# Kernel tuning notes

Measured on AMD Instinct MI355X. Metric: run time of the kernel, lower is better.

Reference implementation:

```python
import jax, jax.numpy as jnp
import numpy as np

NPOINT = 1024
RADII = (0.1, 0.2)
NSAMPLES = (32, 64)
BN_EPS = 1e-5


def _fps(xyz, npoint):
    # furthest point sampling; xyz (B,N,3) -> idx (B,npoint) int32
    B, N, _ = xyz.shape
    def step(carry, _):
        dist, last = carry
        last_pt = jnp.take_along_axis(xyz, last[:, None, None], axis=1)  # (B,1,3)
        d = jnp.sum((xyz - last_pt) ** 2, axis=-1)                       # (B,N)
        dist = jnp.minimum(dist, d)
        nxt = jnp.argmax(dist, axis=1).astype(jnp.int32)
        return (dist, nxt), nxt
    init = (jnp.full((B, N), 1e10, xyz.dtype), jnp.zeros((B,), jnp.int32))
    _, idxs = jax.lax.scan(step, init, None, length=npoint - 1)
    return jnp.concatenate([jnp.zeros((B, 1), jnp.int32), idxs.T], axis=1)


def _ball_query(radius, nsample, xyz, new_xyz):
    # dense ball query: first `nsample` in-radius point indices, pad with first hit
    N = xyz.shape[1]
    d2 = jnp.sum((new_xyz[:, :, None, :] - xyz[:, None, :, :]) ** 2, -1)  # (B,S,N)
    ar = jnp.arange(N, dtype=jnp.int32)
    order = jnp.where(d2 < radius * radius, ar[None, None, :], N)
    idx = -jax.lax.top_k(-order, nsample)[0]          # ascending smallest indices
    first = idx[..., :1]                              # centroid always within radius
    return jnp.where(idx == N, first, idx)


def _group(points, idx):
    # points (B,N,D), idx (B,S,K) -> (B,S,K,D)
    B, S, K = idx.shape
    flat = idx.reshape(B, S * K)
    return jnp.take_along_axis(points, flat[..., None], axis=1).reshape(B, S, K, points.shape[-1])


def _bn(x, g, b, axes):
    # training-mode batch norm over `axes`, channel-last affine
    m = jnp.mean(x, axes, keepdims=True)
    v = jnp.var(x, axes, keepdims=True)
    return g * (x - m) * jax.lax.rsqrt(v + BN_EPS) + b


def setup_inputs() -> dict:
    key = jax.random.key(0)
    ks = jax.random.split(key, 16)
    B, N, C = 8, 4096, 128
    C_in, C_out, mid = 131, 256, 64   # C_in = C + 3 (use_xyz), mid = C_out // 4
    return {
        "xyz": jax.random.uniform(ks[0], (B, N, 3), jnp.float32),
        "features": jax.random.normal(ks[1], (B, C, N), jnp.float32),
        "W1": jax.random.normal(ks[2], (mid, 10), jnp.float32) * 0.3,
        "b1": jnp.zeros((mid,), jnp.float32),
        "W2": jax.random.normal(ks[3], (C_in, mid), jnp.float32) * 0.1,
        "b2": jnp.zeros((C_in,), jnp.float32),
        "Wcr": jax.random.normal(ks[4], (C_out, C_in), jnp.float32) * 0.1,
        "bcr": jnp.zeros((C_out,), jnp.float32),
        "g_map": jax.random.uniform(ks[5], (2, mid), jnp.float32, 0.5, 1.5),
        "b_map": jax.random.normal(ks[6], (2, mid), jnp.float32) * 0.1,
        "g_rs": jax.random.uniform(ks[7], (2, C_in), jnp.float32, 0.5, 1.5),
        "b_rs": jax.random.normal(ks[8], (2, C_in), jnp.float32) * 0.1,
        "g_cr": jax.random.uniform(ks[9], (2, C_out), jnp.float32, 0.5, 1.5),
        "b_cr": jax.random.normal(ks[10], (2, C_out), jnp.float32) * 0.1,
    }


def reference(xyz, features, W1, b1, W2, b2, Wcr, bcr,
              g_map, b_map, g_rs, b_rs, g_cr, b_cr):
    xyz_sg = jax.lax.stop_gradient(xyz)
    fps_idx = _fps(xyz_sg, NPOINT)                                  # (B,S)
    new_xyz = jnp.take_along_axis(xyz, fps_idx[..., None], axis=1)  # (B,S,3)
    pts_feat = jnp.transpose(features, (0, 2, 1))                   # (B,N,C)
    feats_list = []
    for i, (r, k) in enumerate(zip(RADII, NSAMPLES)):
        idx = _ball_query(r, k, xyz_sg, jax.lax.stop_gradient(new_xyz))
        gx = _group(xyz, idx)                      # (B,S,K,3) abs coords
        rel = gx - new_xyz[:, :, None, :]          # (B,S,K,3) relative coords
        gf = _group(pts_feat, idx)                 # (B,S,K,C)
        dist = jnp.sqrt(jnp.sum(rel * rel, -1, keepdims=True) + 1e-12)
        coord_xi = jnp.broadcast_to(gx[:, :, 0:1, :], gx.shape)
        h = jnp.concatenate([dist, coord_xi, gx, rel], axis=-1)     # (B,S,K,10)
        h = jax.nn.relu(_bn(jnp.einsum('bskc,oc->bsko', h, W1) + b1,
                            g_map[i], b_map[i], (0, 1, 2)))
        h = jnp.einsum('bskc,oc->bsko', h, W2) + b2                 # (B,S,K,C_in)
        x = jnp.concatenate([rel, gf], axis=-1)                     # (B,S,K,C_in)
        x = jax.nn.relu(_bn(h * x, g_rs[i], b_rs[i], (0, 1, 2)))
        x = jnp.max(x, axis=2)                                      # pool over nsample
        x = jax.nn.relu(_bn(jnp.einsum('bsc,oc->bso', x, Wcr) + bcr,
                            g_cr[i], b_cr[i], (0, 1)))              # (B,S,C_out)
        feats_list.append(x)
    feats = jnp.transpose(jnp.concatenate(feats_list, -1), (0, 2, 1))  # (B, 2*C_out, S)
    return new_xyz, feats
```

## Files before the change

kernel.cpp:

```cpp
#include <hip/hip_runtime.h>
#include <math.h>

#define NB 8
#define NN 4096
#define NS 1024
#define NC 128
#define MID 64
#define CIN 131
#define COUT 256
#define PSTRIDE (2048 * 262)
#define SSTRIDE (256 * 512)

template <int N>
__device__ __forceinline__ float dpp_ror(float x) {
  return __int_as_float(
      __builtin_amdgcn_update_dpp(0, __float_as_int(x), 0x120 + N, 0xF, 0xF, false));
}
__device__ __forceinline__ float wave_sum(float v) {
  v += dpp_ror<1>(v); v += dpp_ror<2>(v); v += dpp_ror<4>(v); v += dpp_ror<8>(v);
  v += __shfl_xor(v, 16); v += __shfl_xor(v, 32);
  return v;
}
__device__ __forceinline__ float wave_max64(float v) {
  v = fmaxf(v, dpp_ror<1>(v)); v = fmaxf(v, dpp_ror<2>(v));
  v = fmaxf(v, dpp_ror<4>(v)); v = fmaxf(v, dpp_ror<8>(v));
  v = fmaxf(v, __shfl_xor(v, 16)); v = fmaxf(v, __shfl_xor(v, 32));
  return v;
}
__device__ __forceinline__ void wave_sum4(float& a, float& b, float& c, float& d) {
  a += dpp_ror<1>(a); b += dpp_ror<1>(b); c += dpp_ror<1>(c); d += dpp_ror<1>(d);
  a += dpp_ror<2>(a); b += dpp_ror<2>(b); c += dpp_ror<2>(c); d += dpp_ror<2>(d);
  a += dpp_ror<4>(a); b += dpp_ror<4>(b); c += dpp_ror<4>(c); d += dpp_ror<4>(d);
  a += dpp_ror<8>(a); b += dpp_ror<8>(b); c += dpp_ror<8>(c); d += dpp_ror<8>(d);
  a += __shfl_xor(a, 16); b += __shfl_xor(b, 16); c += __shfl_xor(c, 16); d += __shfl_xor(d, 16);
  a += __shfl_xor(a, 32); b += __shfl_xor(b, 32); c += __shfl_xor(c, 32); d += __shfl_xor(d, 32);
}
__device__ __forceinline__ void wave_max4_32(float& a, float& b, float& c, float& d) {
  a = fmaxf(a, dpp_ror<1>(a)); b = fmaxf(b, dpp_ror<1>(b)); c = fmaxf(c, dpp_ror<1>(c)); d = fmaxf(d, dpp_ror<1>(d));
  a = fmaxf(a, dpp_ror<2>(a)); b = fmaxf(b, dpp_ror<2>(b)); c = fmaxf(c, dpp_ror<2>(c)); d = fmaxf(d, dpp_ror<2>(d));
  a = fmaxf(a, dpp_ror<4>(a)); b = fmaxf(b, dpp_ror<4>(b)); c = fmaxf(c, dpp_ror<4>(c)); d = fmaxf(d, dpp_ror<4>(d));
  a = fmaxf(a, dpp_ror<8>(a)); b = fmaxf(b, dpp_ror<8>(b)); c = fmaxf(c, dpp_ror<8>(c)); d = fmaxf(d, dpp_ror<8>(d));
  a = fmaxf(a, __shfl_xor(a, 16)); b = fmaxf(b, __shfl_xor(b, 16));
  c = fmaxf(c, __shfl_xor(c, 16)); d = fmaxf(d, __shfl_xor(d, 16));
}
__device__ __forceinline__ void wave_max4_64(float& a, float& b, float& c, float& d) {
  wave_max4_32(a, b, c, d);
  a = fmaxf(a, __shfl_xor(a, 32)); b = fmaxf(b, __shfl_xor(b, 32));
  c = fmaxf(c, __shfl_xor(c, 32)); d = fmaxf(d, __shfl_xor(d, 32));
}

__global__ __launch_bounds__(256) void fps_kernel(const float* __restrict__ xyz,
                                                  float* __restrict__ out) {
#pragma clang fp contract(off)
  const int b = blockIdx.x;
  const int tid = threadIdx.x;
  const int lane = tid & 63, w = tid >> 6;
  __shared__ float4 pts[NN];
  __shared__ int sel[NS];
  __shared__ unsigned long long wkey[2][4];
  const float* base = xyz + (size_t)b * NN * 3;
  for (int t = tid; t < NN; t += 256)
    pts[t] = make_float4(base[3 * t], base[3 * t + 1], base[3 * t + 2], 0.f);
  if (tid == 0) sel[0] = 0;
  __syncthreads();
  float px[16], py[16], pz[16], dd[16];
#pragma unroll
  for (int q = 0; q < 16; q++) {
    float4 P = pts[tid * 16 + q];
    px[q] = P.x; py[q] = P.y; pz[q] = P.z; dd[q] = 1e10f;
  }
  float lx = pts[0].x, ly = pts[0].y, lz = pts[0].z;
  for (int it = 1; it < NS; ++it) {
    float bv = -1.0f; int bq = 0;
#pragma unroll
    for (int q = 0; q < 16; q++) {
      float dx = px[q] - lx, dy = py[q] - ly, dz = pz[q] - lz;
      float d2 = dx * dx + dy * dy + dz * dz;
      float dn = fminf(dd[q], d2);
      dd[q] = dn;
      if (dn > bv) { bv = dn; bq = q; }
    }
    const int bi = tid * 16 + bq;
    float wm = wave_max64(bv);
    unsigned long long msk = __ballot(bv == wm);
    int srcl = __ffsll(msk) - 1;
    const int p = it & 1;
    if (lane == srcl)
      wkey[p][w] = ((unsigned long long)__float_as_uint(wm) << 32) | (unsigned)(65535 - bi);
    __syncthreads();
    unsigned long long kk = wkey[p][0];
#pragma unroll
    for (int u = 1; u < 4; u++) {
      unsigned long long o = wkey[p][u];
      if (o > kk) kk = o;
    }
    int li = 65535 - (int)(kk & 0xFFFFu);
    if (tid == 0) sel[it] = li;
    float4 L = pts[li];
    lx = L.x; ly = L.y; lz = L.z;
  }
  __syncthreads();
  for (int s = tid; s < NS; s += 256) {
    float4 P = pts[sel[s]];
    float* o = out + ((size_t)b * NS + s) * 3;
    o[0] = P.x; o[1] = P.y; o[2] = P.z;
  }
}

__global__ void ft_kernel(const float* __restrict__ f, float* __restrict__ ft) {
  __shared__ float tile[32][33];
  int n0 = blockIdx.x * 32, c0 = blockIdx.y * 32, b = blockIdx.z;
  int tx = threadIdx.x, ty = threadIdx.y;
  for (int r = 0; r < 32; r += 8)
    tile[ty + r][tx] = f[((size_t)b * NC + (c0 + ty + r)) * NN + n0 + tx];
  __syncthreads();
  for (int r = 0; r < 32; r += 8)
    ft[((size_t)b * NN + n0 + ty + r) * NC + c0 + tx] = tile[tx][ty + r];
}

__global__ void wcrt_kernel(const float* __restrict__ Wcr, float* __restrict__ wcrT) {
  int t = blockIdx.x * blockDim.x + threadIdx.x;
  if (t >= CIN * COUT) return;
  int c = t % COUT, d = t / COUT;
  wcrT[t] = Wcr[c * CIN + d];
}

__global__ __launch_bounds__(256) void ball_kernel(const float* __restrict__ xyz,
                                                   const float* __restrict__ nxyz,
                                                   int* __restrict__ idx0,
                                                   int* __restrict__ idx1) {
#pragma clang fp contract(off)
  __shared__ float4 pts[NN];
  const int scale = blockIdx.y;
  const int K = scale ? 64 : 32;
  const float r2 = scale ? 0.04f : 0.01f;
  int* __restrict__ idx = scale ? idx1 : idx0;
  const int lane = threadIdx.x & 63, w = threadIdx.x >> 6;
  const int c0 = blockIdx.x * 64;
  const int b = c0 >> 10;
  const float* base = xyz + (size_t)b * NN * 3;
  for (int t = threadIdx.x; t < NN; t += 256)
    pts[t] = make_float4(base[3 * t], base[3 * t + 1], base[3 * t + 2], 0.f);
  __syncthreads();
  const unsigned long long ltmask = (1ull << lane) - 1;
  for (int ci = 0; ci < 16; ci++) {
    const int center = c0 + w * 16 + ci;
    const float cx = nxyz[center * 3], cy = nxyz[center * 3 + 1], cz = nxyz[center * 3 + 2];
    int cnt = 0, first = -1;
    int* o = idx + (size_t)center * K;
    for (int st64 = 0; st64 < 64; st64++) {
      const int j = st64 * 64 + lane;
      float4 P = pts[j];
      float dx = P.x - cx, dy = P.y - cy, dz = P.z - cz;
      float d2 = dx * dx + dy * dy + dz * dz;
      const bool hit = d2 < r2;
      unsigned long long mask = __ballot(hit);
      int pos = cnt + __popcll(mask & ltmask);
      if (hit && pos < K) o[pos] = j;
      if (first < 0 && mask) first = st64 * 64 + __ffsll(mask) - 1;
      cnt += __popcll(mask);
      if (cnt >= K) break;
    }
    if (cnt < K && lane >= cnt && lane < K) o[lane] = first;
  }
}

__global__ __launch_bounds__(256) void p1_kernel(
    const float* __restrict__ xyz, const float* __restrict__ nxyz,
    const int* __restrict__ idx0, const int* __restrict__ idx1,
    const float* __restrict__ W1, const float* __restrict__ b1,
    float* __restrict__ parts) {
  __shared__ float accS[MID], accQ[MID];
  const int scale = blockIdx.y;
  const int nblk = scale ? 2048 : 1024;
  if ((int)blockIdx.x >= nblk) return;
  const int K = scale ? 64 : 32, ksh = scale ? 6 : 5, G = scale ? 1 : 2;
  const int* __restrict__ idx = scale ? idx1 : idx0;
  float* __restrict__ partials = parts + (size_t)scale * PSTRIDE + (size_t)blockIdx.x * (2 * MID);
  const int tid = threadIdx.x, lane = tid & 63, wave = tid >> 6;
  if (tid < MID) { accS[tid] = 0.f; accQ[tid] = 0.f; }
  __syncthreads();
  const int sub = lane >> ksh;
  const int k = lane & (K - 1);
  const int center = blockIdx.x * (4 * G) + wave * G + sub;
  const int b = center >> 10;
  const int* ip = idx + (size_t)center * K;
  const int j = ip[k];
  const int j0 = ip[0];
  const float* xb = xyz + (size_t)b * NN * 3;
  const float gxx = xb[3 * j], gxy = xb[3 * j + 1], gxz = xb[3 * j + 2];
  const float c0x = xb[3 * j0], c0y = xb[3 * j0 + 1], c0z = xb[3 * j0 + 2];
  const float cx = nxyz[center * 3], cy = nxyz[center * 3 + 1], cz = nxyz[center * 3 + 2];
  const float rx = gxx - cx, ry = gxy - cy, rz = gxz - cz;
  const float dst = sqrtf(rx * rx + ry * ry + rz * rz + 1e-12f);
  float h[10] = {dst, c0x, c0y, c0z, gxx, gxy, gxz, rx, ry, rz};
#pragma unroll
  for (int c = 0; c < MID; c += 4) {
    float a0 = b1[c], a1 = b1[c + 1], a2 = b1[c + 2], a3 = b1[c + 3];
    const float* w0 = W1 + c * 10;
    const float* w1 = w0 + 10;
    const float* w2 = w0 + 20;
    const float* w3 = w0 + 30;
#pragma unroll
    for (int d = 0; d < 10; d++) {
      a0 += h[d] * w0[d]; a1 += h[d] * w1[d]; a2 += h[d] * w2[d]; a3 += h[d] * w3[d];
    }
    float v0 = a0, v1 = a1, v2 = a2, v3 = a3;
    wave_sum4(v0, v1, v2, v3);
    float q0 = a0 * a0, q1 = a1 * a1, q2 = a2 * a2, q3 = a3 * a3;
    wave_sum4(q0, q1, q2, q3);
    if (lane == 0) {
      atomicAdd(&accS[c], v0); atomicAdd(&accS[c + 1], v1);
      atomicAdd(&accS[c + 2], v2); atomicAdd(&accS[c + 3], v3);
      atomicAdd(&accQ[c], q0); atomicAdd(&accQ[c + 1], q1);
      atomicAdd(&accQ[c + 2], q2); atomicAdd(&accQ[c + 3], q3);
    }
  }
  __syncthreads();
  for (int t = tid; t < 2 * MID; t += 256)
    partials[t] = (t < MID ? accS[t] : accQ[t - MID]);
}

__global__ __launch_bounds__(256) void red2_kernel(const float* __restrict__ pbase,
                                                   int pstride, int nb0, int nb1,
                                                   double* __restrict__ stats, int obase) {
  __shared__ double red[256];
  const int scale = blockIdx.y;
  const int nblk = scale ? nb1 : nb0;
  const float* part = pbase + (size_t)scale * pstride;
  double* st = stats + scale * 1024;
  const int c = blockIdx.x;
  const int ncol = gridDim.x;
  double a = 0.0;
  for (int r = threadIdx.x; r < nblk; r += 256)
    a += (double)part[(size_t)r * ncol + c];
  red[threadIdx.x] = a;
  __syncthreads();
  for (int s = 128; s > 0; s >>= 1) {
    if (threadIdx.x < s) red[threadIdx.x] += red[threadIdx.x + s];
    __syncthreads();
  }
  if (threadIdx.x == 0) st[obase + c] = red[0];
}

template <bool UFT>
__global__ __launch_bounds__(256) void p2_kernel(
    const float* __restrict__ xyz, const float* __restrict__ nxyz,
    const float* __restrict__ feat, const float* __restrict__ ft,
    const int* __restrict__ idx0, const int* __restrict__ idx1,
    const float* __restrict__ W1, const float* __restrict__ b1,
    const float* __restrict__ W2, const float* __restrict__ b2,
    const float* __restrict__ g_map, const float* __restrict__ b_map,
    const double* __restrict__ stats, float* __restrict__ pm0,
    float* __restrict__ pm1, float* __restrict__ parts) {
  __shared__ float accS[CIN], accQ[CIN];
  __shared__ float sc1[MID], sh1[MID];
  const int scale = blockIdx.y;
  const int nblk = scale ? 2048 : 1024;
  if ((int)blockIdx.x >= nblk) return;
  const int K = scale ? 64 : 32, ksh = scale ? 6 : 5, G = scale ? 1 : 2;
  const int* __restrict__ idx = scale ? idx1 : idx0;
  float* __restrict__ pm = scale ? pm1 : pm0;
  const double* st = stats + scale * 1024;
  const float* g1 = g_map + scale * MID;
  const float* bt1 = b_map + scale * MID;
  float* __restrict__ partials = parts + (size_t)scale * PSTRIDE + (size_t)blockIdx.x * (2 * CIN);
  const int tid = threadIdx.x, lane = tid & 63, wave = tid >> 6;
  for (int t = tid; t < CIN; t += 256) { accS[t] = 0.f; accQ[t] = 0.f; }
  if (tid < MID) {
    const double cnt = (double)NB * NS * K;
    double mean = st[tid] / cnt;
    double var = st[64 + tid] / cnt - mean * mean;
    if (var < 0.0) var = 0.0;
    float is = (float)(1.0 / sqrt(var + 1e-5));
    float sc = g1[tid] * is;
    sc1[tid] = sc;
    sh1[tid] = bt1[tid] - (float)mean * sc;
  }
  __syncthreads();
  const int per = nblk >> 3;
  const int lb = ((int)blockIdx.x & 7) * per + ((int)blockIdx.x >> 3);
  const int sub = lane >> ksh;
  const int k = lane & (K - 1);
  const int center = lb * (4 * G) + wave * G + sub;
  const int b = center >> 10;
  const int* ip = idx + (size_t)center * K;
  const int j = ip[k];
  const int j0 = ip[0];
  const float* xb = xyz + (size_t)b * NN * 3;
  const float gxx = xb[3 * j], gxy = xb[3 * j + 1], gxz = xb[3 * j + 2];
  const float c0x = xb[3 * j0], c0y = xb[3 * j0 + 1], c0z = xb[3 * j0 + 2];
  const float cx = nxyz[center * 3], cy = nxyz[center * 3 + 1], cz = nxyz[center * 3 + 2];
  const float rx = gxx - cx, ry = gxy - cy, rz = gxz - cz;
  const float dst = sqrtf(rx * rx + ry * ry + rz * rz + 1e-12f);
  float h[10] = {dst, c0x, c0y, c0z, gxx, gxy, gxz, rx, ry, rz};
  float t[MID];
#pragma unroll
  for (int c = 0; c < MID; c++) {
    float a = b1[c];
    const float* wp = W1 + c * 10;
#pragma unroll
    for (int d = 0; d < 10; d++) a += h[d] * wp[d];
    t[c] = fmaxf(sc1[c] * a + sh1[c], 0.0f);
  }
  auto chan = [&](int c, float x) {
    float z = b2[c];
    const float4* w4 = reinterpret_cast<const float4*>(W2 + c * MID);
#pragma unroll
    for (int d4 = 0; d4 < MID / 4; d4++) {
      float4 w = w4[d4];
      z += t[4 * d4 + 0] * w.x + t[4 * d4 + 1] * w.y + t[4 * d4 + 2] * w.z + t[4 * d4 + 3] * w.w;
    }
    float p = z * x;
    float v = wave_sum(p);
    float q = wave_sum(p * p);
    if (lane == 0) { atomicAdd(&accS[c], v); atomicAdd(&accQ[c], q); }
    float pmax = p;
    if (K == 64) pmax = wave_max64(pmax);
    else {
      pmax = fmaxf(pmax, dpp_ror<1>(pmax)); pmax = fmaxf(pmax, dpp_ror<2>(pmax));
      pmax = fmaxf(pmax, dpp_ror<4>(pmax)); pmax = fmaxf(pmax, dpp_ror<8>(pmax));
      pmax = fmaxf(pmax, __shfl_xor(pmax, 16));
    }
    if (k == (c & (K - 1))) pm[(size_t)center * CIN + c] = pmax;
  };
  auto chan4 = [&](int c, float x0, float x1, float x2, float x3) {
    const float4* wa = reinterpret_cast<const float4*>(W2 + (size_t)(c + 0) * MID);
    const float4* wb = reinterpret_cast<const float4*>(W2 + (size_t)(c + 1) * MID);
    const float4* wc = reinterpret_cast<const float4*>(W2 + (size_t)(c + 2) * MID);
    const float4* wd = reinterpret_cast<const float4*>(W2 + (size_t)(c + 3) * MID);
    float z0 = b2[c], z1 = b2[c + 1], z2 = b2[c + 2], z3 = b2[c + 3];
#pragma unroll
    for (int d4 = 0; d4 < MID / 4; d4++) {
      float t0 = t[4 * d4 + 0], t1 = t[4 * d4 + 1], t2 = t[4 * d4 + 2], t3 = t[4 * d4 + 3];
      float4 w;
      w = wa[d4]; z0 += t0 * w.x + t1 * w.y + t2 * w.z + t3 * w.w;
      w = wb[d4]; z1 += t0 * w.x + t1 * w.y + t2 * w.z + t3 * w.w;
      w = wc[d4]; z2 += t0 * w.x + t1 * w.y + t2 * w.z + t3 * w.w;
      w = wd[d4]; z3 += t0 * w.x + t1 * w.y + t2 * w.z + t3 * w.w;
    }
    float p0 = z0 * x0, p1 = z1 * x1, p2 = z2 * x2, p3 = z3 * x3;
    float v0 = p0, v1 = p1, v2 = p2, v3 = p3;
    wave_sum4(v0, v1, v2, v3);
    float q0 = p0 * p0, q1 = p1 * p1, q2 = p2 * p2, q3 = p3 * p3;
    wave_sum4(q0, q1, q2, q3);
    if (lane == 0) {
      atomicAdd(&accS[c], v0); atomicAdd(&accS[c + 1], v1);
      atomicAdd(&accS[c + 2], v2); atomicAdd(&accS[c + 3], v3);
      atomicAdd(&accQ[c], q0); atomicAdd(&accQ[c + 1], q1);
      atomicAdd(&accQ[c + 2], q2); atomicAdd(&accQ[c + 3], q3);
    }
    float m0 = p0, m1 = p1, m2 = p2, m3 = p3;
    if (K == 64) wave_max4_64(m0, m1, m2, m3);
    else wave_max4_32(m0, m1, m2, m3);
    if (k == ((c + 0) & (K - 1))) pm[(size_t)center * CIN + c + 0] = m0;
    if (k == ((c + 1) & (K - 1))) pm[(size_t)center * CIN + c + 1] = m1;
    if (k == ((c + 2) & (K - 1))) pm[(size_t)center * CIN + c + 2] = m2;
    if (k == ((c + 3) & (K - 1))) pm[(size_t)center * CIN + c + 3] = m3;
  };
  chan(0, rx); chan(1, ry); chan(2, rz);
  const float4* ftb4 = UFT ? reinterpret_cast<const float4*>(ft + ((size_t)b * NN + j) * NC)
                           : nullptr;
  const float* fb = feat + (size_t)b * NC * NN + j;
  for (int f0 = 0; f0 < NC; f0 += 4) {
    float4 fr;
    if (UFT) {
      fr = ftb4[f0 >> 2];
    } else {
      fr.x = fb[(size_t)f0 * NN]; fr.y = fb[(size_t)(f0 + 1) * NN];
      fr.z = fb[(size_t)(f0 + 2) * NN]; fr.w = fb[(size_t)(f0 + 3) * NN];
    }
    chan4(3 + f0, fr.x, fr.y, fr.z, fr.w);
  }
  __syncthreads();
  for (int t = tid; t < 2 * CIN; t += 256)
    partials[t] = (t < CIN ? accS[t] : accQ[t - CIN]);
}

__global__ __launch_bounds__(256) void s4_kernel(const float* __restrict__ pm0,
                                                 const float* __restrict__ pm1,
                                                 const float* __restrict__ wcrT,
                                                 const float* __restrict__ bcr,
                                                 const float* __restrict__ g_rs,
                                                 const float* __restrict__ b_rs,
                                                 float* __restrict__ feats,
                                                 const double* __restrict__ stats,
                                                 float* __restrict__ spart) {
  __shared__ float xms[16][132];
  __shared__ float sc2[CIN], sh2[CIN];
  const int scale = blockIdx.y;
  const int K = scale ? 64 : 32;
  const float* pm = scale ? pm1 : pm0;
  const double* st = stats + scale * 1024;
  const float* g2 = g_rs + scale * CIN;
  const float* bt2 = b_rs + scale * CIN;
  const int choff = scale << 8;
  float* sp = spart + (size_t)scale * SSTRIDE + (size_t)blockIdx.x * 512;
  const int tid = threadIdx.x;
  if (tid < CIN) {
    const double cnt = (double)NB * NS * K;
    double mean = st[128 + tid] / cnt;
    double var = st[259 + tid] / cnt - mean * mean;
    if (var < 0.0) var = 0.0;
    float is = (float)(1.0 / sqrt(var + 1e-5));
    float sc = g2[tid] * is;
    sc2[tid] = sc;
    sh2[tid] = bt2[tid] - (float)mean * sc;
  }
  float bc = bcr[tid];
  float s1 = 0.f, s2 = 0.f;
  __syncthreads();
  for (int r0 = blockIdx.x * 16; r0 < NB * NS; r0 += gridDim.x * 16) {
    for (int t = tid; t < 16 * CIN; t += 256) {
      int rr = t / CIN, cc = t % CIN;
      xms[rr][cc] = fmaxf(sc2[cc] * pm[(size_t)(r0 + rr) * CIN + cc] + sh2[cc], 0.0f);
    }
    __syncthreads();
    float acc[16];
#pragma unroll
    for (int u = 0; u < 16; u++) acc[u] = bc;
    for (int d4 = 0; d4 < 32; d4++) {
      float w0 = wcrT[(4 * d4 + 0) * COUT + tid];
      float w1 = wcrT[(4 * d4 + 1) * COUT + tid];
      float w2 = wcrT[(4 * d4 + 2) * COUT + tid];
      float w3 = wcrT[(4 * d4 + 3) * COUT + tid];
#pragma unroll
      for (int u = 0; u < 16; u++) {
        float4 xv = *reinterpret_cast<const float4*>(&xms[u][4 * d4]);
        acc[u] += xv.x * w0 + xv.y * w1 + xv.z * w2 + xv.w * w3;
      }
    }
#pragma unroll
    for (int d = 128; d < CIN; d++) {
      float w = wcrT[d * COUT + tid];
#pragma unroll
      for (int u = 0; u < 16; u++) acc[u] += xms[u][d] * w;
    }
#pragma unroll
    for (int u = 0; u < 16; u++) {
      int r = r0 + u;
      int b = r >> 10, s = r & (NS - 1);
      feats[((size_t)b * 512 + choff + tid) * NS + s] = acc[u];
      s1 += acc[u];
      s2 += acc[u] * acc[u];
    }
    __syncthreads();
  }
  sp[tid] = s1;
  sp[256 + tid] = s2;
}

__global__ void s5_kernel(float* __restrict__ feats, const double* __restrict__ stats,
                          const float* __restrict__ g_cr, const float* __restrict__ b_cr) {
  const int scale = blockIdx.y;
  const double* st = stats + scale * 1024;
  int t = blockIdx.x * blockDim.x + threadIdx.x;
  int s = t & (NS - 1);
  int c = (t >> 10) & (COUT - 1);
  int b = t >> 18;
  double mean = st[512 + c] / (double)(NB * NS);
  double var = st[768 + c] / (double)(NB * NS) - mean * mean;
  if (var < 0.0) var = 0.0;
  float is = (float)(1.0 / sqrt(var + 1e-5));
  float sc = g_cr[scale * 256 + c] * is;
  float sh = b_cr[scale * 256 + c] - (float)mean * sc;
  size_t o = ((size_t)b * 512 + scale * 256 + c) * NS + s;
  feats[o] = fmaxf(sc * feats[o] + sh, 0.0f);
}

extern "C" void kernel_launch(void* const* d_in, const int* in_sizes, int n_in,
                              void* d_out, int out_size, void* d_ws, size_t ws_size,
                              hipStream_t stream) {
  const float* xyz  = (const float*)d_in[0];
  const float* feat = (const float*)d_in[1];
  const float* W1   = (const float*)d_in[2];
  const float* b1   = (const float*)d_in[3];
  const float* W2   = (const float*)d_in[4];
  const float* b2   = (const float*)d_in[5];
  const float* Wcr  = (const float*)d_in[6];
  const float* bcr  = (const float*)d_in[7];
  const float* g_map = (const float*)d_in[8];
  const float* b_map = (const float*)d_in[9];
  const float* g_rs  = (const float*)d_in[10];
  const float* b_rs  = (const float*)d_in[11];
  const float* g_cr  = (const float*)d_in[12];
  const float* b_cr  = (const float*)d_in[13];

  char* wsb = (char*)d_ws;
  size_t off = 0;
  auto take = [&](size_t bytes) -> void* {
    void* p = wsb + off;
    off = (off + bytes + 255) & ~(size_t)255;
    return p;
  };
  int*    idxb0 = (int*)take((size_t)NB * NS * 32 * sizeof(int));
  int*    idxb1 = (int*)take((size_t)NB * NS * 64 * sizeof(int));
  float*  pm0   = (float*)take((size_t)NB * NS * CIN * sizeof(float));
  float*  pm1   = (float*)take((size_t)NB * NS * CIN * sizeof(float));
  float*  wcrT  = (float*)take((size_t)CIN * COUT * sizeof(float));
  double* stats = (double*)take(2048 * sizeof(double));
  float*  parts = (float*)take((size_t)2 * PSTRIDE * sizeof(float));
  float*  spart = (float*)take((size_t)2 * SSTRIDE * sizeof(float));
  float*  ft    = nullptr;
  if (off + (size_t)NB * NN * NC * sizeof(float) + 256 <= ws_size)
    ft = (float*)take((size_t)NB * NN * NC * sizeof(float));

  float* out = (float*)d_out;
  float* feats = out + NB * NS * 3;

  fps_kernel<<<NB, 256, 0, stream>>>(xyz, out);
  if (ft) ft_kernel<<<dim3(NN / 32, NC / 32, NB), dim3(32, 8), 0, stream>>>(feat, ft);
  wcrt_kernel<<<(CIN * COUT + 255) / 256, 256, 0, stream>>>(Wcr, wcrT);
  ball_kernel<<<dim3(128, 2), 256, 0, stream>>>(xyz, out, idxb0, idxb1);
  p1_kernel<<<dim3(2048, 2), 256, 0, stream>>>(xyz, out, idxb0, idxb1, W1, b1, parts);
  red2_kernel<<<dim3(2 * MID, 2), 256, 0, stream>>>(parts, PSTRIDE, 1024, 2048, stats, 0);
  if (ft)
    p2_kernel<true><<<dim3(2048, 2), 256, 0, stream>>>(xyz, out, feat, ft, idxb0, idxb1,
                                                       W1, b1, W2, b2, g_map, b_map,
                                                       stats, pm0, pm1, parts);
  else
    p2_kernel<false><<<dim3(2048, 2), 256, 0, stream>>>(xyz, out, feat, ft, idxb0, idxb1,
                                                        W1, b1, W2, b2, g_map, b_map,
                                                        stats, pm0, pm1, parts);
  red2_kernel<<<dim3(2 * CIN, 2), 256, 0, stream>>>(parts, PSTRIDE, 1024, 2048, stats, 128);
  s4_kernel<<<dim3(256, 2), 256, 0, stream>>>(pm0, pm1, wcrT, bcr, g_rs, b_rs, feats,
                                              stats, spart);
  red2_kernel<<<dim3(512, 2), 256, 0, stream>>>(spart, SSTRIDE, 256, 256, stats, 512);
  s5_kernel<<<dim3((NB * COUT * NS) / 256, 2), 256, 0, stream>>>(feats, stats, g_cr, b_cr);
  (void)in_sizes; (void)n_in; (void)out_size;
}
```

Measured before the change: 1.300 ms.

## Replace wave-sum reductions with banked LDS atomics and packed FMA math

In the p1 and p2 BN-statistics kernels, the per-channel cross-lane DPP/shuffle sum reductions are replaced by per-lane atomic adds into a 32-column shared-memory array. The columns are summed once at the end of the block. The MLP matvecs in p2 are also rewritten with two-wide float vectors so the compiler can emit packed FMA instructions. This removes many reduction instructions per channel, at the cost of a large LDS footprint (about 33 KB in p2), which may lower occupancy, plus heavy LDS atomic traffic.

```diff
diff --git a/kernel.cpp b/kernel.cpp
--- a/kernel.cpp
+++ b/kernel.cpp
@@ -11,15 +11,12 @@
 #define PSTRIDE (2048 * 262)
 #define SSTRIDE (256 * 512)
 
+typedef float v2f __attribute__((ext_vector_type(2)));
+
 template <int N>
 __device__ __forceinline__ float dpp_ror(float x) {
   return __int_as_float(
       __builtin_amdgcn_update_dpp(0, __float_as_int(x), 0x120 + N, 0xF, 0xF, false));
-}
-__device__ __forceinline__ float wave_sum(float v) {
-  v += dpp_ror<1>(v); v += dpp_ror<2>(v); v += dpp_ror<4>(v); v += dpp_ror<8>(v);
-  v += __shfl_xor(v, 16); v += __shfl_xor(v, 32);
-  return v;
 }
 __device__ __forceinline__ float wave_max64(float v) {
   v = fmaxf(v, dpp_ror<1>(v)); v = fmaxf(v, dpp_ror<2>(v));
@@ -27,13 +24,11 @@
   v = fmaxf(v, __shfl_xor(v, 16)); v = fmaxf(v, __shfl_xor(v, 32));
   return v;
 }
-__device__ __forceinline__ void wave_sum4(float& a, float& b, float& c, float& d) {
-  a += dpp_ror<1>(a); b += dpp_ror<1>(b); c += dpp_ror<1>(c); d += dpp_ror<1>(d);
-  a += dpp_ror<2>(a); b += dpp_ror<2>(b); c += dpp_ror<2>(c); d += dpp_ror<2>(d);
-  a += dpp_ror<4>(a); b += dpp_ror<4>(b); c += dpp_ror<4>(c); d += dpp_ror<4>(d);
-  a += dpp_ror<8>(a); b += dpp_ror<8>(b); c += dpp_ror<8>(c); d += dpp_ror<8>(d);
-  a += __shfl_xor(a, 16); b += __shfl_xor(b, 16); c += __shfl_xor(c, 16); d += __shfl_xor(d, 16);
-  a += __shfl_xor(a, 32); b += __shfl_xor(b, 32); c += __shfl_xor(c, 32); d += __shfl_xor(d, 32);
+__device__ __forceinline__ float wave_max32(float v) {
+  v = fmaxf(v, dpp_ror<1>(v)); v = fmaxf(v, dpp_ror<2>(v));
+  v = fmaxf(v, dpp_ror<4>(v)); v = fmaxf(v, dpp_ror<8>(v));
+  v = fmaxf(v, __shfl_xor(v, 16));
+  return v;
 }
 __device__ __forceinline__ void wave_max4_32(float& a, float& b, float& c, float& d) {
   a = fmaxf(a, dpp_ror<1>(a)); b = fmaxf(b, dpp_ror<1>(b)); c = fmaxf(c, dpp_ror<1>(c)); d = fmaxf(d, dpp_ror<1>(d));
@@ -170,7 +165,8 @@
     const int* __restrict__ idx0, const int* __restrict__ idx1,
     const float* __restrict__ W1, const float* __restrict__ b1,
     float* __restrict__ parts) {
-  __shared__ float accS[MID], accQ[MID];
+  __shared__ float accS2[MID][32];
+  __shared__ float accQ2[MID][32];
   const int scale = blockIdx.y;
   const int nblk = scale ? 2048 : 1024;
   if ((int)blockIdx.x >= nblk) return;
@@ -178,7 +174,10 @@
   const int* __restrict__ idx = scale ? idx1 : idx0;
   float* __restrict__ partials = parts + (size_t)scale * PSTRIDE + (size_t)blockIdx.x * (2 * MID);
   const int tid = threadIdx.x, lane = tid & 63, wave = tid >> 6;
-  if (tid < MID) { accS[tid] = 0.f; accQ[tid] = 0.f; }
+  for (int t = tid; t < MID * 32; t += 256) {
+    ((float*)accS2)[t] = 0.f;
+    ((float*)accQ2)[t] = 0.f;
+  }
   __syncthreads();
   const int sub = lane >> ksh;
   const int k = lane & (K - 1);
@@ -194,6 +193,7 @@
   const float rx = gxx - cx, ry = gxy - cy, rz = gxz - cz;
   const float dst = sqrtf(rx * rx + ry * ry + rz * rz + 1e-12f);
   float h[10] = {dst, c0x, c0y, c0z, gxx, gxy, gxz, rx, ry, rz};
+  const int col = lane & 31;
 #pragma unroll
   for (int c = 0; c < MID; c += 4) {
     float a0 = b1[c], a1 = b1[c + 1], a2 = b1[c + 2], a3 = b1[c + 3];
@@ -205,20 +205,19 @@
     for (int d = 0; d < 10; d++) {
       a0 += h[d] * w0[d]; a1 += h[d] * w1[d]; a2 += h[d] * w2[d]; a3 += h[d] * w3[d];
     }
-    float v0 = a0, v1 = a1, v2 = a2, v3 = a3;
-    wave_sum4(v0, v1, v2, v3);
-    float q0 = a0 * a0, q1 = a1 * a1, q2 = a2 * a2, q3 = a3 * a3;
-    wave_sum4(q0, q1, q2, q3);
-    if (lane == 0) {
-      atomicAdd(&accS[c], v0); atomicAdd(&accS[c + 1], v1);
-      atomicAdd(&accS[c + 2], v2); atomicAdd(&accS[c + 3], v3);
-      atomicAdd(&accQ[c], q0); atomicAdd(&accQ[c + 1], q1);
-      atomicAdd(&accQ[c + 2], q2); atomicAdd(&accQ[c + 3], q3);
-    }
-  }
-  __syncthreads();
-  for (int t = tid; t < 2 * MID; t += 256)
-    partials[t] = (t < MID ? accS[t] : accQ[t - MID]);
+    atomicAdd(&accS2[c + 0][col], a0); atomicAdd(&accS2[c + 1][col], a1);
+    atomicAdd(&accS2[c + 2][col], a2); atomicAdd(&accS2[c + 3][col], a3);
+    atomicAdd(&accQ2[c + 0][col], a0 * a0); atomicAdd(&accQ2[c + 1][col], a1 * a1);
+    atomicAdd(&accQ2[c + 2][col], a2 * a2); atomicAdd(&accQ2[c + 3][col], a3 * a3);
+  }
+  __syncthreads();
+  for (int t = tid; t < 2 * MID; t += 256) {
+    const float* row = (t < MID) ? accS2[t] : accQ2[t - MID];
+    float s = 0.f;
+#pragma unroll
+    for (int i = 0; i < 32; i++) s += row[i];
+    partials[t] = s;
+  }
 }
 
 __global__ __launch_bounds__(256) void red2_kernel(const float* __restrict__ pbase,
@@ -253,7 +252,8 @@
     const float* __restrict__ g_map, const float* __restrict__ b_map,
     const double* __restrict__ stats, float* __restrict__ pm0,
     float* __restrict__ pm1, float* __restrict__ parts) {
-  __shared__ float accS[CIN], accQ[CIN];
+  __shared__ float accS2[CIN][32];
+  __shared__ float accQ2[CIN][32];
   __shared__ float sc1[MID], sh1[MID];
   const int scale = blockIdx.y;
   const int nblk = scale ? 2048 : 1024;
@@ -266,7 +266,10 @@
   const float* bt1 = b_map + scale * MID;
   float* __restrict__ partials = parts + (size_t)scale * PSTRIDE + (size_t)blockIdx.x * (2 * CIN);
   const int tid = threadIdx.x, lane = tid & 63, wave = tid >> 6;
-  for (int t = tid; t < CIN; t += 256) { accS[t] = 0.f; accQ[t] = 0.f; }
+  for (int t = tid; t < CIN * 32; t += 256) {
+    ((float*)accS2)[t] = 0.f;
+    ((float*)accQ2)[t] = 0.f;
+  }
   if (tid < MID) {
     const double cnt = (double)NB * NS * K;
     double mean = st[tid] / cnt;
@@ -294,34 +297,40 @@
   const float rx = gxx - cx, ry = gxy - cy, rz = gxz - cz;
   const float dst = sqrtf(rx * rx + ry * ry + rz * rz + 1e-12f);
   float h[10] = {dst, c0x, c0y, c0z, gxx, gxy, gxz, rx, ry, rz};
-  float t[MID];
-#pragma unroll
-  for (int c = 0; c < MID; c++) {
-    float a = b1[c];
-    const float* wp = W1 + c * 10;
-#pragma unroll
-    for (int d = 0; d < 10; d++) a += h[d] * wp[d];
-    t[c] = fmaxf(sc1[c] * a + sh1[c], 0.0f);
+  const int col = lane & 31;
+  v2f t2[MID / 2];
+#pragma unroll
+  for (int c = 0; c < MID; c += 2) {
+    v2f a = {b1[c], b1[c + 1]};
+    const float* w0 = W1 + c * 10;
+    const float* w1 = w0 + 10;
+#pragma unroll
+    for (int d = 0; d < 10; d++) {
+      v2f wv = {w0[d], w1[d]};
+      v2f hv = {h[d], h[d]};
+      a = hv * wv + a;
+    }
+    v2f sv = {sc1[c], sc1[c + 1]};
+    v2f bv = {sh1[c], sh1[c + 1]};
+    v2f r = sv * a + bv;
+    r[0] = fmaxf(r[0], 0.f); r[1] = fmaxf(r[1], 0.f);
+    t2[c >> 1] = r;
   }
   auto chan = [&](int c, float x) {
-    float z = b2[c];
-    const float4* w4 = reinterpret_cast<const float4*>(W2 + c * MID);
-#pragma unroll
-    for (int d4 = 0; d4 < MID / 4; d4++) {
-      float4 w = w4[d4];
-      z += t[4 * d4 + 0] * w.x + t[4 * d4 + 1] * w.y + t[4 * d4 + 2] * w.z + t[4 * d4 + 3] * w.w;
-    }
+    const float4* w4 = reinterpret_cast<const float4*>(W2 + (size_t)c * MID);
+    v2f zv = {0.f, 0.f};
+#pragma unroll
+    for (int d4 = 0; d4 < 16; d4++) {
+      float4 wq = w4[d4];
+      v2f wlo = {wq.x, wq.y}, whi = {wq.z, wq.w};
+      zv = t2[2 * d4] * wlo + zv;
+      zv = t2[2 * d4 + 1] * whi + zv;
+    }
+    float z = b2[c] + zv[0] + zv[1];
     float p = z * x;
-    float v = wave_sum(p);
-    float q = wave_sum(p * p);
-    if (lane == 0) { atomicAdd(&accS[c], v); atomicAdd(&accQ[c], q); }
-    float pmax = p;
-    if (K == 64) pmax = wave_max64(pmax);
-    else {
-      pmax = fmaxf(pmax, dpp_ror<1>(pmax)); pmax = fmaxf(pmax, dpp_ror<2>(pmax));
-      pmax = fmaxf(pmax, dpp_ror<4>(pmax)); pmax = fmaxf(pmax, dpp_ror<8>(pmax));
-      pmax = fmaxf(pmax, __shfl_xor(pmax, 16));
-    }
+    atomicAdd(&accS2[c][col], p);
+    atomicAdd(&accQ2[c][col], p * p);
+    float pmax = (K == 64) ? wave_max64(p) : wave_max32(p);
     if (k == (c & (K - 1))) pm[(size_t)center * CIN + c] = pmax;
   };
   auto chan4 = [&](int c, float x0, float x1, float x2, float x3) {
@@ -329,27 +338,24 @@
     const float4* wb = reinterpret_cast<const float4*>(W2 + (size_t)(c + 1) * MID);
     const float4* wc = reinterpret_cast<const float4*>(W2 + (size_t)(c + 2) * MID);
     const float4* wd = reinterpret_cast<const float4*>(W2 + (size_t)(c + 3) * MID);
-    float z0 = b2[c], z1 = b2[c + 1], z2 = b2[c + 2], z3 = b2[c + 3];
-#pragma unroll
-    for (int d4 = 0; d4 < MID / 4; d4++) {
-      float t0 = t[4 * d4 + 0], t1 = t[4 * d4 + 1], t2 = t[4 * d4 + 2], t3 = t[4 * d4 + 3];
-      float4 w;
-      w = wa[d4]; z0 += t0 * w.x + t1 * w.y + t2 * w.z + t3 * w.w;
-      w = wb[d4]; z1 += t0 * w.x + t1 * w.y + t2 * w.z + t3 * w.w;
-      w = wc[d4]; z2 += t0 * w.x + t1 * w.y + t2 * w.z + t3 * w.w;
-      w = wd[d4]; z3 += t0 * w.x + t1 * w.y + t2 * w.z + t3 * w.w;
-    }
-    float p0 = z0 * x0, p1 = z1 * x1, p2 = z2 * x2, p3 = z3 * x3;
-    float v0 = p0, v1 = p1, v2 = p2, v3 = p3;
-    wave_sum4(v0, v1, v2, v3);
-    float q0 = p0 * p0, q1 = p1 * p1, q2 = p2 * p2, q3 = p3 * p3;
-    wave_sum4(q0, q1, q2, q3);
-    if (lane == 0) {
-      atomicAdd(&accS[c], v0); atomicAdd(&accS[c + 1], v1);
-      atomicAdd(&accS[c + 2], v2); atomicAdd(&accS[c + 3], v3);
-      atomicAdd(&accQ[c], q0); atomicAdd(&accQ[c + 1], q1);
-      atomicAdd(&accQ[c + 2], q2); atomicAdd(&accQ[c + 3], q3);
-    }
+    v2f z0v = {0.f, 0.f}, z1v = {0.f, 0.f}, z2v = {0.f, 0.f}, z3v = {0.f, 0.f};
+#pragma unroll
+    for (int d4 = 0; d4 < 16; d4++) {
+      v2f tlo = t2[2 * d4], thi = t2[2 * d4 + 1];
+      float4 wq;
+      wq = wa[d4]; { v2f lo = {wq.x, wq.y}, hi = {wq.z, wq.w}; z0v = tlo * lo + z0v; z0v = thi * hi + z0v; }
+      wq = wb[d4]; { v2f lo = {wq.x, wq.y}, hi = {wq.z, wq.w}; z1v = tlo * lo + z1v; z1v = thi * hi + z1v; }
+      wq = wc[d4]; { v2f lo = {wq.x, wq.y}, hi = {wq.z, wq.w}; z2v = tlo * lo + z2v; z2v = thi * hi + z2v; }
+      wq = wd[d4]; { v2f lo = {wq.x, wq.y}, hi = {wq.z, wq.w}; z3v = tlo * lo + z3v; z3v = thi * hi + z3v; }
+    }
+    float p0 = (b2[c + 0] + z0v[0] + z0v[1]) * x0;
+    float p1 = (b2[c + 1] + z1v[0] + z1v[1]) * x1;
+    float p2 = (b2[c + 2] + z2v[0] + z2v[1]) * x2;
+    float p3 = (b2[c + 3] + z3v[0] + z3v[1]) * x3;
+    atomicAdd(&accS2[c + 0][col], p0); atomicAdd(&accS2[c + 1][col], p1);
+    atomicAdd(&accS2[c + 2][col], p2); atomicAdd(&accS2[c + 3][col], p3);
+    atomicAdd(&accQ2[c + 0][col], p0 * p0); atomicAdd(&accQ2[c + 1][col], p1 * p1);
+    atomicAdd(&accQ2[c + 2][col], p2 * p2); atomicAdd(&accQ2[c + 3][col], p3 * p3);
     float m0 = p0, m1 = p1, m2 = p2, m3 = p3;
     if (K == 64) wave_max4_64(m0, m1, m2, m3);
     else wave_max4_32(m0, m1, m2, m3);
@@ -373,8 +379,13 @@
     chan4(3 + f0, fr.x, fr.y, fr.z, fr.w);
   }
   __syncthreads();
-  for (int t = tid; t < 2 * CIN; t += 256)
-    partials[t] = (t < CIN ? accS[t] : accQ[t - CIN]);
+  for (int t = tid; t < 2 * CIN; t += 256) {
+    const float* row = (t < CIN) ? accS2[t] : accQ2[t - CIN];
+    float s = 0.f;
+#pragma unroll
+    for (int i = 0; i < 32; i++) s += row[i];
+    partials[t] = s;
+  }
 }
 
 __global__ __launch_bounds__(256) void s4_kernel(const float* __restrict__ pm0,
```

Result: slower. 2.498 ms (+92.1%).
